# Performance work log

Hardware: AMD Instinct MI355X
Metric: run time of the kernel (lower is better)

Reference implementation:

```python
import jax, jax.numpy as jnp
import numpy as np

EMBED_DIM = 1024
NUM_HEADS = 16
HEAD_DIM = EMBED_DIM // NUM_HEADS
SCALE = float(np.sqrt(HEAD_DIM))


def setup_inputs() -> dict:
    key = jax.random.key(0)
    ks = jax.random.split(key, 7)
    B, S, E = 2, 2048, EMBED_DIM
    query = jax.random.normal(ks[0], (B, S, E), dtype=jnp.float32)
    key_t = jax.random.normal(ks[1], (B, S, E), dtype=jnp.float32)
    value = jax.random.normal(ks[2], (B, S, E), dtype=jnp.float32)
    # nn.Linear(E, E, bias=False): weight shape (out, in); y = x @ W.T
    std = 1.0 / np.sqrt(E)
    Wq = jax.random.uniform(ks[3], (E, E), jnp.float32, -std, std)
    Wk = jax.random.uniform(ks[4], (E, E), jnp.float32, -std, std)
    Wv = jax.random.uniform(ks[5], (E, E), jnp.float32, -std, std)
    Wo = jax.random.uniform(ks[6], (E, E), jnp.float32, -std, std)
    return {"query": query, "key": key_t, "value": value,
            "Wq": Wq, "Wk": Wk, "Wv": Wv, "Wo": Wo}


def reference(query, key, value, Wq, Wk, Wv, Wo):
    B, S, E = query.shape
    H, D = NUM_HEADS, HEAD_DIM
    q = (query @ Wq.T).reshape(B, S, H, D).transpose(0, 2, 1, 3)  # [B,H,S,D]
    k = (key @ Wk.T).reshape(B, S, H, D).transpose(0, 2, 1, 3)
    v = (value @ Wv.T).reshape(B, S, H, D).transpose(0, 2, 1, 3)
    scores = jnp.einsum('bhqd,bhkd->bhqk', q, k) / SCALE  # [B,H,S,S]
    attn = jax.nn.softmax(scores, axis=-1)
    out = jnp.einsum('bhqk,bhkd->bhqd', attn, v)  # [B,H,S,D]
    out = out.transpose(0, 2, 1, 3).reshape(B, S, E)
    return out @ Wo.T
```

## Files before the change

kernel.cpp:

```cpp
#include <hip/hip_runtime.h>
#include <hip/hip_bf16.h>
#include <math.h>

typedef float f32x4 __attribute__((ext_vector_type(4)));
typedef __bf16 bf16x8 __attribute__((ext_vector_type(8)));
typedef unsigned short u16;
typedef u16 u16x8 __attribute__((ext_vector_type(8)));
typedef u16 u16x4 __attribute__((ext_vector_type(4)));
typedef unsigned ui32x4 __attribute__((ext_vector_type(4)));

__device__ __forceinline__ u16 f2bf(float f) {
    unsigned u = __builtin_bit_cast(unsigned, f);
    u = (u + 0x7fffu + ((u >> 16) & 1u)) >> 16;
    return (u16)u;
}
__device__ __forceinline__ unsigned pack2_rhu(float a, float b) {
    return __builtin_amdgcn_perm(__builtin_bit_cast(unsigned, b) + 0x8000u,
                                 __builtin_bit_cast(unsigned, a) + 0x8000u,
                                 0x07060302u);
}
__device__ __forceinline__ unsigned cvtpk(float a, float b) {
    unsigned r;
    asm("v_cvt_pk_bf16_f32 %0, %1, %2" : "=v"(r) : "v"(a), "v"(b));
    return r;
}

#if __has_builtin(__builtin_amdgcn_exp2f)
#define EXP2(x) __builtin_amdgcn_exp2f(x)
#else
#define EXP2(x) exp2f(x)
#endif

__device__ __forceinline__ void gload16(const u16* g, u16* l) {
    __builtin_amdgcn_global_load_lds(
        (const __attribute__((address_space(1))) unsigned int*)(g),
        (__attribute__((address_space(3))) unsigned int*)(l), 16, 0, 0);
}

#if __has_builtin(__builtin_amdgcn_permlane32_swap) && __has_builtin(__builtin_amdgcn_permlane16_swap)
__device__ __forceinline__ void quad_swap(unsigned A, unsigned B, unsigned& dlo,
                                          unsigned& dhi, int quad) {
    auto t = __builtin_amdgcn_permlane32_swap(A, B, false, false);
    auto u = __builtin_amdgcn_permlane16_swap(t[0], t[1], false, false);
    dlo = u[0];
    dhi = u[1];
}
#else
__device__ __forceinline__ void quad_swap(unsigned A, unsigned B, unsigned& dlo,
                                          unsigned& dhi, int quad) {
    unsigned As = (unsigned)__shfl_xor((int)A, 32, 64);
    unsigned Bs = (unsigned)__shfl_xor((int)B, 32, 64);
    unsigned tx = (quad < 2) ? A : Bs;
    unsigned ty = (quad < 2) ? As : B;
    unsigned txs = (unsigned)__shfl_xor((int)tx, 16, 64);
    unsigned tys = (unsigned)__shfl_xor((int)ty, 16, 64);
    dlo = ((quad & 1) == 0) ? tx : tys;
    dhi = ((quad & 1) == 0) ? txs : ty;
}
#endif

__global__ __launch_bounds__(256) void cast_all(
    const float* __restrict__ q, const float* __restrict__ k, const float* __restrict__ v,
    const float* __restrict__ wq, const float* __restrict__ wk, const float* __restrict__ wv,
    const float* __restrict__ wo, u16* __restrict__ dst) {
    int i = blockIdx.x * 256 + threadIdx.x;
    const float* src;
    int off;
    if (i < 3145728) {
        int seg = i >> 20;
        src = (seg == 0) ? q : (seg == 1) ? k : v;
        off = i - (seg << 20);
    } else {
        int j = (i - 3145728) >> 18;
        src = (j == 0) ? wq : (j == 1) ? wk : (j == 2) ? wv : wo;
        off = (i - 3145728) - (j << 18);
    }
    float4 val = ((const float4*)src)[off];
    u16x4 o4;
    o4.x = f2bf(val.x); o4.y = f2bf(val.y); o4.z = f2bf(val.z); o4.w = f2bf(val.w);
    ((u16x4*)dst)[i] = o4;
}

__global__ __launch_bounds__(512) void qkv_gemm(
    const u16* __restrict__ Xq, const u16* __restrict__ Xk, const u16* __restrict__ Xv,
    const u16* __restrict__ Wq, const u16* __restrict__ Wk, const u16* __restrict__ Wv,
    u16* __restrict__ Qo, u16* __restrict__ Ko, u16* __restrict__ Vto) {
    constexpr int K = 1024;
    const int blk = blockIdx.x;
    const int mb = blk & 15;
    const int g = blk >> 4;
    const int z = g >> 3;
    const int nb = g & 7;
    const u16* __restrict__ A = (z == 0) ? Xq : (z == 1) ? Xk : Xv;
    const u16* __restrict__ W = (z == 0) ? Wq : (z == 1) ? Wk : Wv;
    u16* __restrict__ Out = (z == 0) ? Qo : (z == 1) ? Ko : Vto;

    __shared__ __align__(16) u16 Asm[2 * 256 * 64];
    __shared__ __align__(16) u16 Bsm[2 * 128 * 64];

    const int t = threadIdx.x;
    const int lane = t & 63, wave = t >> 6;
    const int quad = lane >> 4, c = lane & 15, cx = c & 7;
    const int wm = wave >> 1, wn = wave & 1;
    const int rowA0 = mb * 256;
    const int colB0 = nb * 128;

    const int l3 = lane >> 3, l7 = lane & 7;
    const int chs = (l7 ^ l3) << 3;
    const u16* gA[4];
    const u16* gB[2];
    int lbA[4];
    int lbB[2];
#pragma unroll
    for (int i = 0; i < 4; ++i) {
        int row = wave * 32 + i * 8 + l3;
        gA[i] = A + (size_t)(rowA0 + row) * K + chs;
        lbA[i] = (wave * 32 + i * 8) * 64;
    }
#pragma unroll
    for (int i = 0; i < 2; ++i) {
        int row = wave * 16 + i * 8 + l3;
        gB[i] = W + (size_t)(colB0 + row) * K + chs;
        lbB[i] = (wave * 16 + i * 8) * 64;
    }

    const f32x4 zero4 = {0.f, 0.f, 0.f, 0.f};
    f32x4 acc[4][4];
#pragma unroll
    for (int i = 0; i < 4; ++i)
#pragma unroll
        for (int j = 0; j < 4; ++j) acc[i][j] = zero4;

#pragma unroll
    for (int i = 0; i < 4; ++i) gload16(gA[i], Asm + lbA[i]);
#pragma unroll
    for (int i = 0; i < 2; ++i) gload16(gB[i], Bsm + lbB[i]);
#pragma unroll
    for (int i = 0; i < 4; ++i) gload16(gA[i] + 64, Asm + 16384 + lbA[i]);
#pragma unroll
    for (int i = 0; i < 2; ++i) gload16(gB[i] + 64, Bsm + 8192 + lbB[i]);
    asm volatile("s_waitcnt vmcnt(6)" ::: "memory");
    __builtin_amdgcn_s_barrier();
    asm volatile("" ::: "memory");

    for (int kt = 0; kt < 16; ++kt) {
        const int cur = kt & 1;
        const u16* Ab = Asm + cur * 16384;
        const u16* Bb = Bsm + cur * 8192;
#pragma unroll
        for (int ks = 0; ks < 2; ++ks) {
            const int co = ((ks * 4 + quad) ^ cx) << 3;
            bf16x8 af[4], bfr[4];
#pragma unroll
            for (int mi = 0; mi < 4; ++mi)
                af[mi] = *(const bf16x8*)(Ab + (wm * 64 + mi * 16 + c) * 64 + co);
#pragma unroll
            for (int nj = 0; nj < 4; ++nj)
                bfr[nj] = *(const bf16x8*)(Bb + (wn * 64 + nj * 16 + c) * 64 + co);
            if (ks == 1) {
                asm volatile("s_waitcnt lgkmcnt(0)" ::: "memory");
                __builtin_amdgcn_s_barrier();
                asm volatile("" ::: "memory");
                if (kt + 2 < 16) {
                    const int koff = (kt + 2) * 64;
                    u16* ab = Asm + cur * 16384;
                    u16* bb = Bsm + cur * 8192;
#pragma unroll
                    for (int i = 0; i < 4; ++i) gload16(gA[i] + koff, ab + lbA[i]);
#pragma unroll
                    for (int i = 0; i < 2; ++i) gload16(gB[i] + koff, bb + lbB[i]);
                }
            }
            __builtin_amdgcn_s_setprio(1);
            if (z == 2) {
#pragma unroll
                for (int mi = 0; mi < 4; ++mi)
#pragma unroll
                    for (int nj = 0; nj < 4; ++nj)
                        acc[mi][nj] = __builtin_amdgcn_mfma_f32_16x16x32_bf16(bfr[nj], af[mi], acc[mi][nj], 0, 0, 0);
            } else {
#pragma unroll
                for (int mi = 0; mi < 4; ++mi)
#pragma unroll
                    for (int nj = 0; nj < 4; ++nj)
                        acc[mi][nj] = __builtin_amdgcn_mfma_f32_16x16x32_bf16(af[mi], bfr[nj], acc[mi][nj], 0, 0, 0);
            }
            __builtin_amdgcn_s_setprio(0);
        }
        if (kt <= 13) {
            asm volatile("s_waitcnt vmcnt(6)" ::: "memory");
        } else {
            asm volatile("s_waitcnt vmcnt(0)" ::: "memory");
        }
        __builtin_amdgcn_s_barrier();
        asm volatile("" ::: "memory");
    }

    const float scale = (z == 0) ? 0.18033688011112042f : 1.0f;
#pragma unroll
    for (int mi = 0; mi < 4; ++mi) {
#pragma unroll
        for (int nj = 0; nj < 4; ++nj) {
#pragma unroll
            for (int r = 0; r < 4; ++r) {
                float v = acc[mi][nj][r];
                if (z == 2) {
                    int n = colB0 + wn * 64 + nj * 16 + quad * 4 + r;
                    int m = rowA0 + wm * 64 + mi * 16 + c;
                    int b = m >> 11, s = m & 2047, h = n >> 6, d = n & 63;
                    Out[((((b << 4) | h) << 6) + d) * 2048 + s] = f2bf(v);
                } else {
                    int m = rowA0 + wm * 64 + mi * 16 + quad * 4 + r;
                    int n = colB0 + wn * 64 + nj * 16 + c;
                    int b = m >> 11, s = m & 2047, h = n >> 6, d = n & 63;
                    Out[((((b << 4) | h) * 2048 + s) << 6) + d] = f2bf(v * scale);
                }
            }
        }
    }
}

__global__ __launch_bounds__(256, 2) void out_gemm(const u16* __restrict__ A,
                                                   const u16* __restrict__ W,
                                                   float* __restrict__ Out) {
    constexpr int K = 1024;
    __shared__ __align__(16) u16 As[64 * 64];
    __shared__ __align__(16) u16 Bs[128 * 64];
    const int blk = blockIdx.x;
    const int yb = blk & 63;
    const int xb = blk >> 6;
    const int t = threadIdx.x;
    const int lane = t & 63, wave = t >> 6;
    const int quad = lane >> 4, c = lane & 15, cx = c & 7;
    const int wr = (wave >> 1) * 32, wc = (wave & 1) * 64;
    const int rowA0 = yb * 64;
    const int colB0 = xb * 128;

    const int l3 = lane >> 3, l7 = lane & 7;
    const int chs = (l7 ^ l3) << 3;
    const u16* gA[2];
    const u16* gB[4];
    u16* lA[2];
    u16* lB[4];
#pragma unroll
    for (int i = 0; i < 2; ++i) {
        int row = wave * 16 + i * 8 + l3;
        gA[i] = A + (size_t)(rowA0 + row) * K + chs;
        lA[i] = As + (wave * 128 + i * 64) * 8;
    }
#pragma unroll
    for (int i = 0; i < 4; ++i) {
        int row = wave * 32 + i * 8 + l3;
        gB[i] = W + (size_t)(colB0 + row) * K + chs;
        lB[i] = Bs + (wave * 256 + i * 64) * 8;
    }

    const f32x4 zero4 = {0.f, 0.f, 0.f, 0.f};
    f32x4 acc[2][4];
#pragma unroll
    for (int i = 0; i < 2; ++i)
#pragma unroll
        for (int j = 0; j < 4; ++j) acc[i][j] = zero4;

    for (int kt = 0; kt < K; kt += 64) {
        __syncthreads();
#pragma unroll
        for (int i = 0; i < 2; ++i) gload16(gA[i] + kt, lA[i]);
#pragma unroll
        for (int i = 0; i < 4; ++i) gload16(gB[i] + kt, lB[i]);
        __syncthreads();
#pragma unroll
        for (int ks = 0; ks < 2; ++ks) {
            const int co = ((ks * 4 + quad) ^ cx) << 3;
            bf16x8 af[2], bfr[4];
#pragma unroll
            for (int i = 0; i < 2; ++i)
                af[i] = *(const bf16x8*)(As + (wr + i * 16 + c) * 64 + co);
#pragma unroll
            for (int j = 0; j < 4; ++j)
                bfr[j] = *(const bf16x8*)(Bs + (wc + j * 16 + c) * 64 + co);
#pragma unroll
            for (int i = 0; i < 2; ++i)
#pragma unroll
                for (int j = 0; j < 4; ++j)
                    acc[i][j] = __builtin_amdgcn_mfma_f32_16x16x32_bf16(af[i], bfr[j], acc[i][j], 0, 0, 0);
        }
    }
#pragma unroll
    for (int i = 0; i < 2; ++i)
#pragma unroll
        for (int j = 0; j < 4; ++j)
#pragma unroll
            for (int r = 0; r < 4; ++r) {
                int m = rowA0 + wr + i * 16 + quad * 4 + r;
                int n = colB0 + wc + j * 16 + c;
                Out[(m << 10) + n] = acc[i][j][r];
            }
}

__global__ __launch_bounds__(512, 4) void flash_attn(const u16* __restrict__ Qp,
                                                     const u16* __restrict__ Kp,
                                                     const u16* __restrict__ Vt,
                                                     u16* __restrict__ Ob) {
    constexpr int S = 2048;
    const int blk = blockIdx.x;
    const int j = blk & 31;
    const int bh = ((j & 7) << 2) | (j >> 3);
    const int b = bh >> 4, h = bh & 15;
    const int t = threadIdx.x, wave = t >> 6, lane = t & 63;
    const int wq = wave & 3, kh = wave >> 2;
    const int quad = lane >> 4, c = lane & 15, cx = c & 7;
    const int qw = (blk >> 5) * 128 + wq * 32;
    const u16* Qb = Qp + (bh * S + qw) * 64;
    const u16* Kb = Kp + (bh * S + kh * 1024) * 64;
    const u16* Vb = Vt + bh * 64 * S + kh * 1024;

    __shared__ __align__(16) u16 smem[32768];
    u16* const Kh = smem + kh * 8192;
    u16* const Vh = smem + 16384 + kh * 8192;

    bf16x8 qf[2][2];
#pragma unroll
    for (int qt = 0; qt < 2; ++qt)
#pragma unroll
        for (int hf = 0; hf < 2; ++hf)
            qf[qt][hf] = *(const bf16x8*)(Qb + (qt * 16 + c) * 64 + hf * 32 + quad * 8);

    u16x8 ou;
#pragma unroll
    for (int i = 0; i < 8; ++i) ou[i] = 0x3F80;
    const bf16x8 onesf = __builtin_bit_cast(bf16x8, ou);

    const int l3 = lane >> 3, l7 = lane & 7;
    const int chs = (l7 ^ l3) << 3;
    const u16* gK[2];
    const u16* gV[2];
    int lbase[2];
#pragma unroll
    for (int i = 0; i < 2; ++i) {
        int row = wq * 16 + i * 8 + l3;
        gK[i] = Kb + row * 64 + chs;
        gV[i] = Vb + row * 2048 + chs;
        lbase[i] = (wq * 128 + i * 64) * 8;
    }
#pragma unroll
    for (int i = 0; i < 2; ++i) {
        gload16(gK[i], Kh + lbase[i]);
        gload16(gV[i], Vh + lbase[i]);
    }
    __syncthreads();

    const f32x4 zero4 = {0.f, 0.f, 0.f, 0.f};
    f32x4 o[2][4];
    f32x4 ol[2];
#pragma unroll
    for (int qt = 0; qt < 2; ++qt) {
        ol[qt] = zero4;
#pragma unroll
        for (int t2 = 0; t2 < 4; ++t2) o[qt][t2] = zero4;
    }

    const int co0 = (quad ^ cx) << 3, co1 = ((4 + quad) ^ cx) << 3;

    for (int it = 0; it < 16; ++it) {
        const int cur = it & 1;
        if (it + 1 < 16) {
#pragma unroll
            for (int i = 0; i < 2; ++i) {
                gload16(gK[i] + (it + 1) * 4096, Kh + (cur ^ 1) * 4096 + lbase[i]);
                gload16(gV[i] + (it + 1) * 64, Vh + (cur ^ 1) * 4096 + lbase[i]);
            }
        }
        const u16* Kc = Kh + cur * 4096;
        const u16* Vc = Vh + cur * 4096;
        f32x4 sc[4][2];
        __builtin_amdgcn_s_setprio(1);
#pragma unroll
        for (int kt = 0; kt < 4; ++kt) {
            const int krow = (kt * 16 + c) * 64;
            bf16x8 kf0 = *(const bf16x8*)(Kc + krow + co0);
            bf16x8 kf1 = *(const bf16x8*)(Kc + krow + co1);
#pragma unroll
            for (int qt = 0; qt < 2; ++qt) {
                f32x4 zz = zero4;
                zz = __builtin_amdgcn_mfma_f32_16x16x32_bf16(kf0, qf[qt][0], zz, 0, 0, 0);
                zz = __builtin_amdgcn_mfma_f32_16x16x32_bf16(kf1, qf[qt][1], zz, 0, 0, 0);
                sc[kt][qt] = zz;
            }
        }
        __builtin_amdgcn_s_setprio(0);
        bf16x8 af[2][2];
#pragma unroll
        for (int qt = 0; qt < 2; ++qt) {
            unsigned dw[4][2];
#pragma unroll
            for (int kt = 0; kt < 4; ++kt) {
                dw[kt][0] = cvtpk(EXP2(sc[kt][qt][0]), EXP2(sc[kt][qt][1]));
                dw[kt][1] = cvtpk(EXP2(sc[kt][qt][2]), EXP2(sc[kt][qt][3]));
            }
#pragma unroll
            for (int hh = 0; hh < 2; ++hh) {
                unsigned d0, d1, d2, d3;
                quad_swap(dw[2 * hh][0], dw[2 * hh + 1][0], d0, d2, quad);
                quad_swap(dw[2 * hh][1], dw[2 * hh + 1][1], d1, d3, quad);
                ui32x4 dd = {d0, d1, d2, d3};
                af[qt][hh] = __builtin_bit_cast(bf16x8, dd);
            }
        }
        __builtin_amdgcn_s_setprio(1);
#pragma unroll
        for (int qt = 0; qt < 2; ++qt) {
            ol[qt] = __builtin_amdgcn_mfma_f32_16x16x32_bf16(af[qt][0], onesf, ol[qt], 0, 0, 0);
            ol[qt] = __builtin_amdgcn_mfma_f32_16x16x32_bf16(af[qt][1], onesf, ol[qt], 0, 0, 0);
        }
#pragma unroll
        for (int t2 = 0; t2 < 4; ++t2) {
            const int vrow = (t2 * 16 + c) * 64;
            bf16x8 vf0 = *(const bf16x8*)(Vc + vrow + co0);
            bf16x8 vf1 = *(const bf16x8*)(Vc + vrow + co1);
#pragma unroll
            for (int qt = 0; qt < 2; ++qt) {
                o[qt][t2] = __builtin_amdgcn_mfma_f32_16x16x32_bf16(af[qt][0], vf0, o[qt][t2], 0, 0, 0);
                o[qt][t2] = __builtin_amdgcn_mfma_f32_16x16x32_bf16(af[qt][1], vf1, o[qt][t2], 0, 0, 0);
            }
        }
        __builtin_amdgcn_s_setprio(0);
        __syncthreads();
    }
    float* const cb = ((float*)smem) + ((wq << 6) | lane) * 41;
    if (kh == 1) {
        int idx = 0;
#pragma unroll
        for (int qt = 0; qt < 2; ++qt)
#pragma unroll
            for (int t2 = 0; t2 < 4; ++t2)
#pragma unroll
                for (int r = 0; r < 4; ++r) cb[idx++] = o[qt][t2][r];
#pragma unroll
        for (int qt = 0; qt < 2; ++qt)
#pragma unroll
            for (int r = 0; r < 4; ++r) cb[idx++] = ol[qt][r];
    }
    __syncthreads();
    if (kh == 0) {
        int idx = 0;
#pragma unroll
        for (int qt = 0; qt < 2; ++qt)
#pragma unroll
            for (int t2 = 0; t2 < 4; ++t2)
#pragma unroll
                for (int r = 0; r < 4; ++r) o[qt][t2][r] += cb[idx++];
#pragma unroll
        for (int qt = 0; qt < 2; ++qt)
#pragma unroll
            for (int r = 0; r < 4; ++r) ol[qt][r] += cb[idx++];
#pragma unroll
        for (int qt = 0; qt < 2; ++qt)
#pragma unroll
            for (int r = 0; r < 4; ++r) {
                float inv = 1.f / ol[qt][r];
                int row = qw + qt * 16 + quad * 4 + r;
                int base = ((b * S + row) * 16 + h) * 64;
#pragma unroll
                for (int t2 = 0; t2 < 4; ++t2)
                    Ob[base + t2 * 16 + c] = f2bf(o[qt][t2][r] * inv);
            }
    }
}

extern "C" void kernel_launch(void* const* d_in, const int* in_sizes, int n_in,
                              void* d_out, int out_size, void* d_ws, size_t ws_size,
                              hipStream_t stream) {
    const float* q  = (const float*)d_in[0];
    const float* k  = (const float*)d_in[1];
    const float* v  = (const float*)d_in[2];
    const float* wq = (const float*)d_in[3];
    const float* wk = (const float*)d_in[4];
    const float* wv = (const float*)d_in[5];
    const float* wo = (const float*)d_in[6];

    u16* ws = (u16*)d_ws;
    u16* qb  = ws;
    u16* kb  = ws + 4194304;
    u16* vb  = ws + 8388608;
    u16* wqb = ws + 12582912;
    u16* wkb = ws + 13631488;
    u16* wvb = ws + 14680064;
    u16* wob = ws + 15728640;
    u16* Qp  = ws + 16777216;
    u16* Kp  = ws + 20971520;
    u16* Vtp = ws + 25165824;
    u16* Obf = ws + 29360128;

    cast_all<<<16384, 256, 0, stream>>>(q, k, v, wq, wk, wv, wo, ws);

    qkv_gemm<<<384, 512, 0, stream>>>(qb, kb, vb, wqb, wkb, wvb, Qp, Kp, Vtp);

    flash_attn<<<512, 512, 0, stream>>>(Qp, Kp, Vtp, Obf);

    out_gemm<<<512, 256, 0, stream>>>(Obf, wob, (float*)d_out);
}
```

Baseline: 204.0 us.

## Double-buffer out_gemm with 128x128 tiles and 512-thread blocks

Rewrites the output projection GEMM to use 128x128 block tiles with 8 waves and 256 blocks, and a two-stage LDS double buffer. Global-to-LDS loads for tile kt+2 are issued while the current tile is being consumed, gated by explicit vmcnt waits and barriers, with raised priority around the MFMA bursts. The goal is to overlap memory latency with compute and to reuse more operand data per block. The trade-off is fewer blocks (256) relative to CU count and higher LDS use per block.

```diff
diff --git a/kernel.cpp b/kernel.cpp
--- a/kernel.cpp
+++ b/kernel.cpp
@@ -13,11 +13,6 @@
     unsigned u = __builtin_bit_cast(unsigned, f);
     u = (u + 0x7fffu + ((u >> 16) & 1u)) >> 16;
     return (u16)u;
-}
-__device__ __forceinline__ unsigned pack2_rhu(float a, float b) {
-    return __builtin_amdgcn_perm(__builtin_bit_cast(unsigned, b) + 0x8000u,
-                                 __builtin_bit_cast(unsigned, a) + 0x8000u,
-                                 0x07060302u);
 }
 __device__ __forceinline__ unsigned cvtpk(float a, float b) {
     unsigned r;
@@ -220,81 +215,111 @@
     }
 }
 
-__global__ __launch_bounds__(256, 2) void out_gemm(const u16* __restrict__ A,
-                                                   const u16* __restrict__ W,
-                                                   float* __restrict__ Out) {
+__global__ __launch_bounds__(512) void out_gemm(const u16* __restrict__ A,
+                                                const u16* __restrict__ W,
+                                                float* __restrict__ Out) {
     constexpr int K = 1024;
-    __shared__ __align__(16) u16 As[64 * 64];
-    __shared__ __align__(16) u16 Bs[128 * 64];
+    __shared__ __align__(16) u16 Asm[2 * 128 * 64];
+    __shared__ __align__(16) u16 Bsm[2 * 128 * 64];
     const int blk = blockIdx.x;
-    const int yb = blk & 63;
-    const int xb = blk >> 6;
+    const int mb = blk & 31;
+    const int nb = blk >> 5;
     const int t = threadIdx.x;
     const int lane = t & 63, wave = t >> 6;
     const int quad = lane >> 4, c = lane & 15, cx = c & 7;
-    const int wr = (wave >> 1) * 32, wc = (wave & 1) * 64;
-    const int rowA0 = yb * 64;
-    const int colB0 = xb * 128;
+    const int wm = wave >> 2, wn = wave & 3;
+    const int rowA0 = mb * 128;
+    const int colB0 = nb * 128;
 
     const int l3 = lane >> 3, l7 = lane & 7;
     const int chs = (l7 ^ l3) << 3;
     const u16* gA[2];
-    const u16* gB[4];
-    u16* lA[2];
-    u16* lB[4];
+    const u16* gB[2];
+    int lb[2];
 #pragma unroll
     for (int i = 0; i < 2; ++i) {
         int row = wave * 16 + i * 8 + l3;
         gA[i] = A + (size_t)(rowA0 + row) * K + chs;
-        lA[i] = As + (wave * 128 + i * 64) * 8;
-    }
-#pragma unroll
-    for (int i = 0; i < 4; ++i) {
-        int row = wave * 32 + i * 8 + l3;
         gB[i] = W + (size_t)(colB0 + row) * K + chs;
-        lB[i] = Bs + (wave * 256 + i * 64) * 8;
+        lb[i] = (wave * 16 + i * 8) * 64;
     }
 
     const f32x4 zero4 = {0.f, 0.f, 0.f, 0.f};
-    f32x4 acc[2][4];
-#pragma unroll
-    for (int i = 0; i < 2; ++i)
-#pragma unroll
-        for (int j = 0; j < 4; ++j) acc[i][j] = zero4;
-
-    for (int kt = 0; kt < K; kt += 64) {
-        __syncthreads();
-#pragma unroll
-        for (int i = 0; i < 2; ++i) gload16(gA[i] + kt, lA[i]);
-#pragma unroll
-        for (int i = 0; i < 4; ++i) gload16(gB[i] + kt, lB[i]);
-        __syncthreads();
+    f32x4 acc[4][2];
+#pragma unroll
+    for (int i = 0; i < 4; ++i)
+#pragma unroll
+        for (int j = 0; j < 2; ++j) acc[i][j] = zero4;
+
+#pragma unroll
+    for (int i = 0; i < 2; ++i) {
+        gload16(gA[i], Asm + lb[i]);
+        gload16(gB[i], Bsm + lb[i]);
+    }
+#pragma unroll
+    for (int i = 0; i < 2; ++i) {
+        gload16(gA[i] + 64, Asm + 8192 + lb[i]);
+        gload16(gB[i] + 64, Bsm + 8192 + lb[i]);
+    }
+    asm volatile("s_waitcnt vmcnt(4)" ::: "memory");
+    __builtin_amdgcn_s_barrier();
+    asm volatile("" ::: "memory");
+
+    for (int kt = 0; kt < 16; ++kt) {
+        const int cur = kt & 1;
+        const u16* Ab = Asm + cur * 8192;
+        const u16* Bb = Bsm + cur * 8192;
 #pragma unroll
         for (int ks = 0; ks < 2; ++ks) {
             const int co = ((ks * 4 + quad) ^ cx) << 3;
-            bf16x8 af[2], bfr[4];
-#pragma unroll
-            for (int i = 0; i < 2; ++i)
-                af[i] = *(const bf16x8*)(As + (wr + i * 16 + c) * 64 + co);
-#pragma unroll
-            for (int j = 0; j < 4; ++j)
-                bfr[j] = *(const bf16x8*)(Bs + (wc + j * 16 + c) * 64 + co);
-#pragma unroll
-            for (int i = 0; i < 2; ++i)
-#pragma unroll
-                for (int j = 0; j < 4; ++j)
-                    acc[i][j] = __builtin_amdgcn_mfma_f32_16x16x32_bf16(af[i], bfr[j], acc[i][j], 0, 0, 0);
-        }
-    }
-#pragma unroll
-    for (int i = 0; i < 2; ++i)
-#pragma unroll
-        for (int j = 0; j < 4; ++j)
+            bf16x8 af[4], bfr[2];
+#pragma unroll
+            for (int mi = 0; mi < 4; ++mi)
+                af[mi] = *(const bf16x8*)(Ab + (wm * 64 + mi * 16 + c) * 64 + co);
+#pragma unroll
+            for (int nj = 0; nj < 2; ++nj)
+                bfr[nj] = *(const bf16x8*)(Bb + (wn * 32 + nj * 16 + c) * 64 + co);
+            if (ks == 1) {
+                asm volatile("s_waitcnt lgkmcnt(0)" ::: "memory");
+                __builtin_amdgcn_s_barrier();
+                asm volatile("" ::: "memory");
+                if (kt + 2 < 16) {
+                    const int koff = (kt + 2) * 64;
+                    u16* ab = Asm + cur * 8192;
+                    u16* bb = Bsm + cur * 8192;
+#pragma unroll
+                    for (int i = 0; i < 2; ++i) {
+                        gload16(gA[i] + koff, ab + lb[i]);
+                        gload16(gB[i] + koff, bb + lb[i]);
+                    }
+                }
+            }
+            __builtin_amdgcn_s_setprio(1);
+#pragma unroll
+            for (int mi = 0; mi < 4; ++mi)
+#pragma unroll
+                for (int nj = 0; nj < 2; ++nj)
+                    acc[mi][nj] = __builtin_amdgcn_mfma_f32_16x16x32_bf16(af[mi], bfr[nj], acc[mi][nj], 0, 0, 0);
+            __builtin_amdgcn_s_setprio(0);
+        }
+        if (kt <= 13) {
+            asm volatile("s_waitcnt vmcnt(4)" ::: "memory");
+        } else {
+            asm volatile("s_waitcnt vmcnt(0)" ::: "memory");
+        }
+        __builtin_amdgcn_s_barrier();
+        asm volatile("" ::: "memory");
+    }
+
+#pragma unroll
+    for (int mi = 0; mi < 4; ++mi)
+#pragma unroll
+        for (int nj = 0; nj < 2; ++nj)
 #pragma unroll
             for (int r = 0; r < 4; ++r) {
-                int m = rowA0 + wr + i * 16 + quad * 4 + r;
-                int n = colB0 + wc + j * 16 + c;
-                Out[(m << 10) + n] = acc[i][j][r];
+                int m = rowA0 + wm * 64 + mi * 16 + quad * 4 + r;
+                int n = colB0 + wn * 32 + nj * 16 + c;
+                Out[(m << 10) + n] = acc[mi][nj][r];
             }
 }
 
@@ -498,5 +523,5 @@
 
     flash_attn<<<512, 512, 0, stream>>>(Qp, Kp, Vtp, Obf);
 
-    out_gemm<<<512, 256, 0, stream>>>(Obf, wob, (float*)d_out);
-}
+    out_gemm<<<256, 512, 0, stream>>>(Obf, wob, (float*)d_out);
+}
```

Measured after the change: 205.2 us, median of 2. No clear change (+0.6%).
